# Performance work log

Measured on AMD Instinct MI355X. Metric: run time of the kernel, lower is better.

The kernel has to match this reference:

```python
import jax, jax.numpy as jnp
import numpy as np

N_BIT = 4
GROUP = 128
ALPHA_W = 1.0   # group_size > -1 forces weight alpha to 1.0
ALPHA_A = 0.9   # searched input alpha
TOKENS, D_IN, D_OUT = 2048, 2048, 2048


def _int_grid(n_bit):
    B = n_bit - 1
    v = [0.0] + [float(s * i) for i in range(1, 2 ** B) for s in (1, -1)]
    v = np.sort(np.asarray(v, np.float32)) * (32.0 / 2 ** B)
    return v


def _outlier_grid(n_bit, exp_bit=2, exp_base=5):
    B = n_bit - 1
    mant_bit = B - exp_bit
    vals = []
    for i in range(exp_base, exp_base + 2 ** exp_bit):
        for j in range(2 ** mant_bit):
            if i == exp_base and j == 0:
                continue
            v = 2.0 ** i * (1.0 + 2.0 ** (-mant_bit) * j)
            vals += [v, -v]
    return np.sort(np.asarray(vals, np.float32))


_QG = _int_grid(N_BIT)
MAX_Q = float(_QG.max())              # 28.0 for 4-bit int grid
MERGED_GRID = jnp.asarray(np.concatenate([_QG, _outlier_grid(N_BIT)]))  # [29]


def get_quant(x, alpha, group_size):
    """Faithful jax port of get_quant(): per-group scale, nearest merged-grid
    quantization, roll-based outlier/victim masking, fp16 dequant."""
    org_shape = x.shape
    if group_size == -2:
        t = x.reshape(-1)
        mean, std = t.mean(), t.std(ddof=1)
    else:
        t = x.reshape(-1, group_size) if group_size > 0 else x
        mean = t.mean(axis=1, keepdims=True)
        std = t.std(axis=1, ddof=1, keepdims=True)
    normal_max = jnp.maximum(jnp.abs(mean + 3 * std), jnp.abs(mean - 3 * std))
    scales = normal_max * alpha / MAX_Q
    # nearest grid point over merged quant+outlier grid (the chunk loop in the
    # original is memory-chunking only; math is identical done whole)
    labels = jnp.argmin(jnp.abs((t / scales)[..., None] - MERGED_GRID), axis=-1)
    qf = MERGED_GRID[labels].reshape(-1)
    # victim masking: outliers (|q|>32) steal their paired neighbor's slot
    mask = jnp.abs(qf) > 32.0
    victim_odd = jnp.roll(mask, 1).at[::2].set(False)
    victim_even = jnp.roll(mask & ~victim_odd, -1).at[1::2].set(False)
    qf = jnp.where(victim_odd | victim_even, 0.0, qf)
    if group_size >= -1:
        qf = qf.reshape(t.shape)
    deq = (qf * scales).astype(jnp.float16)
    return deq.reshape(org_shape)


def setup_inputs() -> dict:
    key = jax.random.key(0)
    k1, k2 = jax.random.split(key)
    x = jax.random.normal(k1, (TOKENS, D_IN), dtype=jnp.float32)
    weight = jax.random.normal(k2, (D_OUT, D_IN), dtype=jnp.float32) * 0.02
    return {"x": x, "weight": weight}


def reference(x, weight):
    # runtime path of OliVe_Linear.forward (post-calibration), group_size=128
    w_deq = get_quant(weight, ALPHA_W, GROUP).astype(jnp.float32)
    x_deq = get_quant(x, ALPHA_A, GROUP).astype(jnp.float32)
    return x_deq @ w_deq.T  # [tokens, out_features]
```

## Files before the change

### kernel.cpp

```cpp
#include <hip/hip_runtime.h>
#include <hip/hip_fp16.h>
#include <stdint.h>

#define TOKENS 2048
#define DIM    2048
#define GROUP  128
#define NGK    16

typedef __attribute__((ext_vector_type(4)))  int   i32x4;
typedef __attribute__((ext_vector_type(16))) int   i32x16;
typedef __attribute__((ext_vector_type(4)))  float f32x4;
typedef __attribute__((ext_vector_type(16))) float f32x16;


__device__ __forceinline__ float group32_sum(float v) {
#pragma unroll
  for (int off = 16; off > 0; off >>= 1)
    v += __shfl_xor(v, off, 64);
  return v;
}

__device__ __forceinline__ float nearest_q4(float u) {
  float qi = fminf(fmaxf(rintf(u), -7.f), 7.f);
  float a = fabsf(u);
  float m = a <= 14.f ? 12.f : a <= 20.f ? 16.f : a <= 28.f ? 24.f
          : a <= 40.f ? 32.f : a <= 56.f ? 48.f : a <= 80.f ? 64.f : 96.f;
  float qo = copysignf(m, u);
  return (fabsf(u - qo) < fabsf(u - qi)) ? qo : qi;
}

__global__ __launch_bounds__(256) void quant2_kernel(
    const float* __restrict__ x, const float* __restrict__ w,
    int8_t* __restrict__ q8,
    float* __restrict__ ssxT,
    float* __restrict__ sswT) {
  const int wid  = threadIdx.x >> 6;
  const int lane = threadIdx.x & 63;
  const int l    = lane & 31;
  const int g    = blockIdx.x * 8 + wid * 2 + (lane >> 5);
  const int NG1  = TOKENS * DIM / GROUP;

  const float alpha = (g < NG1) ? 0.9f : 1.0f;
  const float* src  = (g < NG1) ? x : w;
  const int grow    = (g < NG1) ? g : g - NG1;
  const size_t sbase = (size_t)grow * GROUP + l * 4;

  const float4 v = *reinterpret_cast<const float4*>(src + sbase);

  const float mean = group32_sum(v.x + v.y + v.z + v.w) * (1.0f / 128.0f);
  const float d0 = v.x - mean, d1 = v.y - mean, d2 = v.z - mean, d3 = v.w - mean;
  const float var = group32_sum(d0 * d0 + d1 * d1 + d2 * d2 + d3 * d3) *
                    (1.0f / 127.0f);
  const float scale = (fabsf(mean) + 3.0f * sqrtf(var)) * alpha / 28.0f;
  const float rs4 = 0.25f / scale;

  float q0 = nearest_q4(v.x * rs4);
  float q1 = nearest_q4(v.y * rs4);
  float q2 = nearest_q4(v.z * rs4);
  float q3 = nearest_q4(v.w * rs4);
  if (fabsf(q0) > 8.0f)      q1 = 0.0f;
  else if (fabsf(q1) > 8.0f) q0 = 0.0f;
  if (fabsf(q2) > 8.0f)      q3 = 0.0f;
  else if (fabsf(q3) > 8.0f) q2 = 0.0f;

  const int p = ((int)q0 & 255) | (((int)q1 & 255) << 8) |
                (((int)q2 & 255) << 16) | (((int)q3 & 255) << 24);
  reinterpret_cast<int*>(q8)[(size_t)g * 32 + l] = p;

  if (l == 0) {
    const float ss = 4.0f * scale;
    if (g < NG1) ssxT[(grow & 15) * 2048 + (grow >> 4)] = ss;
    else         sswT[(grow & 15) * 2048 + (grow >> 4)] = ss;
  }
}


__device__ __forceinline__ void gload_lds16(const int8_t* g, char* l) {
  __builtin_amdgcn_global_load_lds(
      (__attribute__((address_space(1))) uint32_t*)g,
      (__attribute__((address_space(3))) uint32_t*)l, 16, 0, 0);
}

__global__ __launch_bounds__(256, 2) void gemm_kernel(
    const int8_t* __restrict__ Aq, const int8_t* __restrict__ Bq,
    const float* __restrict__ ssxT, const float* __restrict__ sswT,
    float* __restrict__ C) {
  __shared__ char lds_raw[2 * 24576 + 12288];
  float* ssx_l = (float*)(lds_raw + 49152);
  float* ssw_l = (float*)(lds_raw + 49152 + 8192);

  const int tid  = threadIdx.x;
  const int lane = tid & 63;
  const int wid  = tid >> 6;
  const int wr   = wid >> 1;
  const int wc   = wid & 1;
  const int r31  = lane & 31;
  const int hi   = lane >> 5;

  const int bid = blockIdx.x;
  const int c   = bid & 7;
  const int idx = bid >> 3;
  const int bm  = ((c & 3) << 2) + (idx >> 4);
  const int bn  = ((c >> 2) << 4) + (idx & 15);

  const int8_t* gA = Aq + (size_t)(bm * 128) * DIM;
  const int8_t* gB = Bq + (size_t)(bn * 64) * DIM;

  auto stage = [&](char* buf, int g) {
#pragma unroll
    for (int i = 0; i < 4; ++i) {
      int P   = (i * 256 + tid) * 16;
      int row = P >> 7;
      int cb  = (P & 127) ^ ((row & 7) << 4);
      gload_lds16(gA + (size_t)row * DIM + g * 128 + cb, buf + P);
    }
#pragma unroll
    for (int i = 0; i < 2; ++i) {
      int P   = (i * 256 + tid) * 16;
      int row = P >> 7;
      int cb  = (P & 127) ^ ((row & 7) << 4);
      gload_lds16(gB + (size_t)row * DIM + g * 128 + cb, buf + 16384 + P);
    }
  };

#pragma unroll
  for (int i = 0; i < 2; ++i) {
    int f = (i * 256 + tid) * 4;
    *reinterpret_cast<f32x4*>(&ssx_l[f]) =
        *reinterpret_cast<const f32x4*>(&ssxT[(f >> 7) * 2048 + bm * 128 + (f & 127)]);
  }
  {
    int f = tid * 4;
    *reinterpret_cast<f32x4*>(&ssw_l[f]) =
        *reinterpret_cast<const f32x4*>(&sswT[(f >> 6) * 2048 + bn * 64 + (f & 63)]);
  }
  __syncthreads();

  f32x16 accf[2] = {};
  const i32x16 zacc = {};

  auto compute = [&](const char* buf, int gk) {
    const char* cA = buf;
    const char* cB = buf + 16384;
    i32x16 acci[2];
#pragma unroll
    for (int ks = 0; ks < 4; ++ks) {
      const int cb = ks * 32 + hi * 16;
      i32x4 af[2], bf;
#pragma unroll
      for (int mt = 0; mt < 2; ++mt) {
        int row = wr * 64 + mt * 32 + r31;
        int pc  = cb ^ ((row & 7) << 4);
        af[mt] = *reinterpret_cast<const i32x4*>(cA + (row << 7) + pc);
      }
      {
        int row = wc * 32 + r31;
        int pc  = cb ^ ((row & 7) << 4);
        bf = *reinterpret_cast<const i32x4*>(cB + (row << 7) + pc);
      }
      __builtin_amdgcn_s_setprio(1);
#pragma unroll
      for (int mt = 0; mt < 2; ++mt)
        acci[mt] = __builtin_amdgcn_mfma_i32_32x32x32_i8(
            af[mt], bf, ks == 0 ? zacc : acci[mt], 0, 0, 0);
      __builtin_amdgcn_s_setprio(0);
    }
    const float sw = ssw_l[gk * 64 + wc * 32 + r31];
#pragma unroll
    for (int mt = 0; mt < 2; ++mt)
#pragma unroll
      for (int q = 0; q < 4; ++q) {
        f32x4 sx = *reinterpret_cast<const f32x4*>(
            &ssx_l[gk * 128 + wr * 64 + mt * 32 + 8 * q + 4 * hi]);
#pragma unroll
        for (int e = 0; e < 4; ++e)
          accf[mt][q * 4 + e] += sx[e] * (sw * (float)acci[mt][q * 4 + e]);
      }
  };

  char* S0 = lds_raw;
  char* S1 = lds_raw + 24576;

  stage(S0, 0);
#pragma unroll 2
  for (int j = 0; j < NGK; ++j) {
    if (j + 1 < NGK) {
      stage((j & 1) ? S0 : S1, j + 1);
      asm volatile("s_waitcnt vmcnt(6)" ::: "memory");
    } else {
      asm volatile("s_waitcnt vmcnt(0)" ::: "memory");
    }
    __builtin_amdgcn_s_barrier();
    compute((j & 1) ? S1 : S0, j);
    __builtin_amdgcn_s_barrier();
  }

  const int crow0 = bm * 128 + wr * 64 + 4 * hi;
  const int ccol  = bn * 64 + wc * 32 + r31;
#pragma unroll
  for (int mt = 0; mt < 2; ++mt)
#pragma unroll
    for (int r = 0; r < 16; ++r) {
      int row = crow0 + mt * 32 + (r & 3) + 8 * (r >> 2);
      C[(size_t)row * DIM + ccol] = accf[mt][r];
    }
}


extern "C" void kernel_launch(void* const* d_in, const int* in_sizes, int n_in,
                              void* d_out, int out_size, void* d_ws,
                              size_t ws_size, hipStream_t stream) {
  const float* x = (const float*)d_in[0];
  const float* w = (const float*)d_in[1];
  float* out = (float*)d_out;

  int8_t* qx   = (int8_t*)d_ws;
  int8_t* qw   = qx + (size_t)TOKENS * DIM;
  float*  ssxT = (float*)(qw + (size_t)DIM * DIM);
  float*  sswT = ssxT + NGK * 2048;

  const int ngroups = 2 * TOKENS * DIM / GROUP;
  quant2_kernel<<<ngroups / 8, 256, 0, stream>>>(x, w, qx, ssxT, sswT);

  gemm_kernel<<<512, 256, 0, stream>>>(qx, qw, ssxT, sswT, out);
}
```

Before: 33.94 us.

## Split GEMM K-steps across wave pairs with LDS reduction of partial tiles

Each of the two column waves now covers the full 64-column tile but only half of the K-steps per group (intra-K split). Each wave holds four accumulator tiles and applies the per-group scales to its own partial sums. The partials are then reduced through LDS before one wave writes the output. This reuses each A fragment across two B tiles, cutting LDS reads per MFMA. In exchange it doubles accumulator registers, which may reduce occupancy, and adds an epilogue reduction with barriers. It also drops the unroll-by-2 hint on the main loop.

```diff
diff --git a/kernel.cpp b/kernel.cpp
--- a/kernel.cpp
+++ b/kernel.cpp
@@ -93,7 +93,7 @@
   const int lane = tid & 63;
   const int wid  = tid >> 6;
   const int wr   = wid >> 1;
-  const int wc   = wid & 1;
+  const int wz   = wid & 1;
   const int r31  = lane & 31;
   const int hi   = lane >> 5;
 
@@ -136,36 +136,43 @@
   }
   __syncthreads();
 
-  f32x16 accf[2] = {};
+  f32x16 accf[2][2] = {};
   const i32x16 zacc = {};
 
   auto compute = [&](const char* buf, int gk) {
     const char* cA = buf;
     const char* cB = buf + 16384;
-    i32x16 acci[2];
-#pragma unroll
-    for (int ks = 0; ks < 4; ++ks) {
+    i32x16 acci[2][2];
+#pragma unroll
+    for (int s = 0; s < 2; ++s) {
+      const int ks = wz * 2 + s;
       const int cb = ks * 32 + hi * 16;
-      i32x4 af[2], bf;
+      i32x4 af[2], bf[2];
 #pragma unroll
       for (int mt = 0; mt < 2; ++mt) {
         int row = wr * 64 + mt * 32 + r31;
         int pc  = cb ^ ((row & 7) << 4);
         af[mt] = *reinterpret_cast<const i32x4*>(cA + (row << 7) + pc);
       }
-      {
-        int row = wc * 32 + r31;
+#pragma unroll
+      for (int nt = 0; nt < 2; ++nt) {
+        int row = nt * 32 + r31;
         int pc  = cb ^ ((row & 7) << 4);
-        bf = *reinterpret_cast<const i32x4*>(cB + (row << 7) + pc);
+        bf[nt] = *reinterpret_cast<const i32x4*>(cB + (row << 7) + pc);
       }
       __builtin_amdgcn_s_setprio(1);
 #pragma unroll
       for (int mt = 0; mt < 2; ++mt)
-        acci[mt] = __builtin_amdgcn_mfma_i32_32x32x32_i8(
-            af[mt], bf, ks == 0 ? zacc : acci[mt], 0, 0, 0);
+#pragma unroll
+        for (int nt = 0; nt < 2; ++nt)
+          acci[mt][nt] = __builtin_amdgcn_mfma_i32_32x32x32_i8(
+              af[mt], bf[nt], s == 0 ? zacc : acci[mt][nt], 0, 0, 0);
       __builtin_amdgcn_s_setprio(0);
     }
-    const float sw = ssw_l[gk * 64 + wc * 32 + r31];
+    float sw[2];
+#pragma unroll
+    for (int nt = 0; nt < 2; ++nt)
+      sw[nt] = ssw_l[gk * 64 + nt * 32 + r31];
 #pragma unroll
     for (int mt = 0; mt < 2; ++mt)
 #pragma unroll
@@ -173,8 +180,11 @@
         f32x4 sx = *reinterpret_cast<const f32x4*>(
             &ssx_l[gk * 128 + wr * 64 + mt * 32 + 8 * q + 4 * hi]);
 #pragma unroll
-        for (int e = 0; e < 4; ++e)
-          accf[mt][q * 4 + e] += sx[e] * (sw * (float)acci[mt][q * 4 + e]);
+        for (int nt = 0; nt < 2; ++nt)
+#pragma unroll
+          for (int e = 0; e < 4; ++e)
+            accf[mt][nt][q * 4 + e] +=
+                sx[e] * (sw[nt] * (float)acci[mt][nt][q * 4 + e]);
       }
   };
 
@@ -182,7 +192,6 @@
   char* S1 = lds_raw + 24576;
 
   stage(S0, 0);
-#pragma unroll 2
   for (int j = 0; j < NGK; ++j) {
     if (j + 1 < NGK) {
       stage((j & 1) ? S0 : S1, j + 1);
@@ -195,15 +204,52 @@
     __builtin_amdgcn_s_barrier();
   }
 
-  const int crow0 = bm * 128 + wr * 64 + 4 * hi;
-  const int ccol  = bn * 64 + wc * 32 + r31;
-#pragma unroll
-  for (int mt = 0; mt < 2; ++mt)
-#pragma unroll
-    for (int r = 0; r < 16; ++r) {
-      int row = crow0 + mt * 32 + (r & 3) + 8 * (r >> 2);
-      C[(size_t)row * DIM + ccol] = accf[mt][r];
-    }
+  __syncthreads();
+  float* red = (float*)lds_raw;
+  if (wz == 1) {
+#pragma unroll
+    for (int mt = 0; mt < 2; ++mt)
+#pragma unroll
+      for (int nt = 0; nt < 2; ++nt) {
+        const int t = mt * 2 + nt;
+#pragma unroll
+        for (int q = 0; q < 4; ++q) {
+          f32x4 v;
+          v.x = accf[mt][nt][q * 4 + 0];
+          v.y = accf[mt][nt][q * 4 + 1];
+          v.z = accf[mt][nt][q * 4 + 2];
+          v.w = accf[mt][nt][q * 4 + 3];
+          *reinterpret_cast<f32x4*>(
+              red + (size_t)((wr * 16 + t * 4 + q) * 64 + lane) * 4) = v;
+        }
+      }
+  }
+  __syncthreads();
+  if (wz == 0) {
+    const int crow0 = bm * 128 + wr * 64 + 4 * hi;
+    const int ccol0 = bn * 64 + r31;
+#pragma unroll
+    for (int mt = 0; mt < 2; ++mt)
+#pragma unroll
+      for (int nt = 0; nt < 2; ++nt) {
+        const int t = mt * 2 + nt;
+#pragma unroll
+        for (int q = 0; q < 4; ++q) {
+          f32x4 v = *reinterpret_cast<const f32x4*>(
+              red + (size_t)((wr * 16 + t * 4 + q) * 64 + lane) * 4);
+          accf[mt][nt][q * 4 + 0] += v.x;
+          accf[mt][nt][q * 4 + 1] += v.y;
+          accf[mt][nt][q * 4 + 2] += v.z;
+          accf[mt][nt][q * 4 + 3] += v.w;
+        }
+#pragma unroll
+        for (int r = 0; r < 16; ++r) {
+          int row = crow0 + mt * 32 + (r & 3) + 8 * (r >> 2);
+          int col = ccol0 + nt * 32;
+          C[(size_t)row * DIM + col] = accf[mt][nt][r];
+        }
+      }
+  }
 }
 
 
```

Measured after the change: 37.74 us. +11.2%, slower.

## Triple-buffer GEMM LDS pipeline and store group scales as fp16

Applied to the files above, without the earlier changes.

Changes the int8 GEMM main loop from double to triple buffering, issuing loads two K-groups ahead and waiting with vmcnt(12). This hides more global-load latency. To fit three 24 KB stages in LDS, the per-group scales are stored and staged as fp16 instead of fp32, which halves the scale footprint. The costs are rounding error in the scales and higher LDS use per block (about 78 KB), which may limit occupancy under the 2-block launch bound.

```diff
diff --git a/kernel.cpp b/kernel.cpp
--- a/kernel.cpp
+++ b/kernel.cpp
@@ -7,6 +7,9 @@
 #define GROUP  128
 #define NGK    16
 
+typedef _Float16 half_t;
+typedef __attribute__((ext_vector_type(4)))  _Float16 f16x4;
+typedef __attribute__((ext_vector_type(8)))  _Float16 f16x8;
 typedef __attribute__((ext_vector_type(4)))  int   i32x4;
 typedef __attribute__((ext_vector_type(16))) int   i32x16;
 typedef __attribute__((ext_vector_type(4)))  float f32x4;
@@ -32,8 +35,8 @@
 __global__ __launch_bounds__(256) void quant2_kernel(
     const float* __restrict__ x, const float* __restrict__ w,
     int8_t* __restrict__ q8,
-    float* __restrict__ ssxT,
-    float* __restrict__ sswT) {
+    half_t* __restrict__ ssxT,
+    half_t* __restrict__ sswT) {
   const int wid  = threadIdx.x >> 6;
   const int lane = threadIdx.x & 63;
   const int l    = lane & 31;
@@ -68,7 +71,7 @@
   reinterpret_cast<int*>(q8)[(size_t)g * 32 + l] = p;
 
   if (l == 0) {
-    const float ss = 4.0f * scale;
+    const half_t ss = (half_t)(4.0f * scale);
     if (g < NG1) ssxT[(grow & 15) * 2048 + (grow >> 4)] = ss;
     else         sswT[(grow & 15) * 2048 + (grow >> 4)] = ss;
   }
@@ -83,11 +86,11 @@
 
 __global__ __launch_bounds__(256, 2) void gemm_kernel(
     const int8_t* __restrict__ Aq, const int8_t* __restrict__ Bq,
-    const float* __restrict__ ssxT, const float* __restrict__ sswT,
+    const half_t* __restrict__ ssxT, const half_t* __restrict__ sswT,
     float* __restrict__ C) {
-  __shared__ char lds_raw[2 * 24576 + 12288];
-  float* ssx_l = (float*)(lds_raw + 49152);
-  float* ssw_l = (float*)(lds_raw + 49152 + 8192);
+  __shared__ char lds_raw[3 * 24576 + 6144];
+  half_t* ssx_l = (half_t*)(lds_raw + 73728);
+  half_t* ssw_l = (half_t*)(lds_raw + 73728 + 4096);
 
   const int tid  = threadIdx.x;
   const int lane = tid & 63;
@@ -123,16 +126,15 @@
     }
   };
 
-#pragma unroll
-  for (int i = 0; i < 2; ++i) {
-    int f = (i * 256 + tid) * 4;
-    *reinterpret_cast<f32x4*>(&ssx_l[f]) =
-        *reinterpret_cast<const f32x4*>(&ssxT[(f >> 7) * 2048 + bm * 128 + (f & 127)]);
-  }
   {
-    int f = tid * 4;
-    *reinterpret_cast<f32x4*>(&ssw_l[f]) =
-        *reinterpret_cast<const f32x4*>(&sswT[(f >> 6) * 2048 + bn * 64 + (f & 63)]);
+    int f = tid * 8;
+    *reinterpret_cast<f16x8*>(&ssx_l[f]) =
+        *reinterpret_cast<const f16x8*>(&ssxT[(f >> 7) * 2048 + bm * 128 + (f & 127)]);
+  }
+  if (tid < 128) {
+    int f = tid * 8;
+    *reinterpret_cast<f16x8*>(&ssw_l[f]) =
+        *reinterpret_cast<const f16x8*>(&sswT[(f >> 6) * 2048 + bn * 64 + (f & 63)]);
   }
   __syncthreads();
 
@@ -165,35 +167,50 @@
             af[mt], bf, ks == 0 ? zacc : acci[mt], 0, 0, 0);
       __builtin_amdgcn_s_setprio(0);
     }
-    const float sw = ssw_l[gk * 64 + wc * 32 + r31];
+    const float sw = (float)ssw_l[gk * 64 + wc * 32 + r31];
 #pragma unroll
     for (int mt = 0; mt < 2; ++mt)
 #pragma unroll
       for (int q = 0; q < 4; ++q) {
-        f32x4 sx = *reinterpret_cast<const f32x4*>(
+        f16x4 sxh = *reinterpret_cast<const f16x4*>(
             &ssx_l[gk * 128 + wr * 64 + mt * 32 + 8 * q + 4 * hi]);
 #pragma unroll
         for (int e = 0; e < 4; ++e)
-          accf[mt][q * 4 + e] += sx[e] * (sw * (float)acci[mt][q * 4 + e]);
+          accf[mt][q * 4 + e] +=
+              (float)sxh[e] * (sw * (float)acci[mt][q * 4 + e]);
       }
   };
 
   char* S0 = lds_raw;
   char* S1 = lds_raw + 24576;
+  char* S2 = lds_raw + 49152;
 
   stage(S0, 0);
-#pragma unroll 2
-  for (int j = 0; j < NGK; ++j) {
-    if (j + 1 < NGK) {
-      stage((j & 1) ? S0 : S1, j + 1);
+  stage(S1, 1);
+
+  auto iter = [&](int j, const char* cbuf, char* sbuf) {
+    if (j <= 13) {
+      stage(sbuf, j + 2);
+      asm volatile("s_waitcnt vmcnt(12)" ::: "memory");
+    } else if (j == 14) {
       asm volatile("s_waitcnt vmcnt(6)" ::: "memory");
     } else {
       asm volatile("s_waitcnt vmcnt(0)" ::: "memory");
     }
     __builtin_amdgcn_s_barrier();
-    compute((j & 1) ? S1 : S0, j);
+    compute(cbuf, j);
     __builtin_amdgcn_s_barrier();
-  }
+  };
+
+  for (int t = 0; t < 12; t += 3) {
+    iter(t + 0, S0, S2);
+    iter(t + 1, S1, S0);
+    iter(t + 2, S2, S1);
+  }
+  iter(12, S0, S2);
+  iter(13, S1, S0);
+  iter(14, S2, S1);
+  iter(15, S0, S2);
 
   const int crow0 = bm * 128 + wr * 64 + 4 * hi;
   const int ccol  = bn * 64 + wc * 32 + r31;
@@ -216,8 +233,8 @@
 
   int8_t* qx   = (int8_t*)d_ws;
   int8_t* qw   = qx + (size_t)TOKENS * DIM;
-  float*  ssxT = (float*)(qw + (size_t)DIM * DIM);
-  float*  sswT = ssxT + NGK * 2048;
+  half_t* ssxT = (half_t*)(qw + (size_t)DIM * DIM);
+  half_t* sswT = ssxT + NGK * 2048;
 
   const int ngroups = 2 * TOKENS * DIM / GROUP;
   quant2_kernel<<<ngroups / 8, 256, 0, stream>>>(x, w, qx, ssxT, sswT);
```

Result: slower. 35.51 us (+4.6%).

## Software-pipeline group-scale epilogue behind next group's MFMAs, batch LDS fragment loads

Applied to the files above, without the earlier changes.

Restructures the GEMM main loop so each k-group's int32 accumulators are scaled and added into the float accumulators during the following iteration, alternating between two accumulator sets. It also loads all four k-slices of A/B fragments from LDS up front before issuing the MFMAs. The aim is to overlap the dequant-scale FMAs and LDS fragment latency with MFMA execution instead of serializing them. This costs more registers (two i32x16 pairs, cached scales, 12 fragment vectors), which may pressure occupancy at launch bounds of 2 waves per SIMD.

```diff
diff --git a/kernel.cpp b/kernel.cpp
--- a/kernel.cpp
+++ b/kernel.cpp
@@ -139,51 +139,24 @@
   f32x16 accf[2] = {};
   const i32x16 zacc = {};
 
-  auto compute = [&](const char* buf, int gk) {
-    const char* cA = buf;
-    const char* cB = buf + 16384;
-    i32x16 acci[2];
-#pragma unroll
-    for (int ks = 0; ks < 4; ++ks) {
-      const int cb = ks * 32 + hi * 16;
-      i32x4 af[2], bf;
-#pragma unroll
-      for (int mt = 0; mt < 2; ++mt) {
-        int row = wr * 64 + mt * 32 + r31;
-        int pc  = cb ^ ((row & 7) << 4);
-        af[mt] = *reinterpret_cast<const i32x4*>(cA + (row << 7) + pc);
-      }
-      {
-        int row = wc * 32 + r31;
-        int pc  = cb ^ ((row & 7) << 4);
-        bf = *reinterpret_cast<const i32x4*>(cB + (row << 7) + pc);
-      }
-      __builtin_amdgcn_s_setprio(1);
-#pragma unroll
-      for (int mt = 0; mt < 2; ++mt)
-        acci[mt] = __builtin_amdgcn_mfma_i32_32x32x32_i8(
-            af[mt], bf, ks == 0 ? zacc : acci[mt], 0, 0, 0);
-      __builtin_amdgcn_s_setprio(0);
-    }
-    const float sw = ssw_l[gk * 64 + wc * 32 + r31];
-#pragma unroll
-    for (int mt = 0; mt < 2; ++mt)
-#pragma unroll
-      for (int q = 0; q < 4; ++q) {
-        f32x4 sx = *reinterpret_cast<const f32x4*>(
-            &ssx_l[gk * 128 + wr * 64 + mt * 32 + 8 * q + 4 * hi]);
-#pragma unroll
-        for (int e = 0; e < 4; ++e)
-          accf[mt][q * 4 + e] += sx[e] * (sw * (float)acci[mt][q * 4 + e]);
-      }
-  };
-
   char* S0 = lds_raw;
   char* S1 = lds_raw + 24576;
 
-  stage(S0, 0);
-#pragma unroll 2
-  for (int j = 0; j < NGK; ++j) {
+  float sw_c = 0.0f;
+  f32x4 sx_c[2][4];
+
+  auto apply = [&](const i32x16 prev[2]) {
+#pragma unroll
+    for (int mt = 0; mt < 2; ++mt)
+#pragma unroll
+      for (int q = 0; q < 4; ++q)
+#pragma unroll
+        for (int e = 0; e < 4; ++e)
+          accf[mt][q * 4 + e] +=
+              sx_c[mt][q][e] * (sw_c * (float)prev[mt][q * 4 + e]);
+  };
+
+  auto step = [&](int j, i32x16 out[2], const i32x16 prev[2]) {
     if (j + 1 < NGK) {
       stage((j & 1) ? S0 : S1, j + 1);
       asm volatile("s_waitcnt vmcnt(6)" ::: "memory");
@@ -191,9 +164,54 @@
       asm volatile("s_waitcnt vmcnt(0)" ::: "memory");
     }
     __builtin_amdgcn_s_barrier();
-    compute((j & 1) ? S1 : S0, j);
+    const char* buf = (j & 1) ? S1 : S0;
+    const char* cA = buf;
+    const char* cB = buf + 16384;
+
+    i32x4 af[4][2], bf[4];
+#pragma unroll
+    for (int ks = 0; ks < 4; ++ks) {
+      const int cb = ks * 32 + hi * 16;
+#pragma unroll
+      for (int mt = 0; mt < 2; ++mt) {
+        int row = wr * 64 + mt * 32 + r31;
+        int pc  = cb ^ ((row & 7) << 4);
+        af[ks][mt] = *reinterpret_cast<const i32x4*>(cA + (row << 7) + pc);
+      }
+      int row = wc * 32 + r31;
+      int pc  = cb ^ ((row & 7) << 4);
+      bf[ks] = *reinterpret_cast<const i32x4*>(cB + (row << 7) + pc);
+    }
+
+    if (j > 0) apply(prev);
+
+    sw_c = ssw_l[j * 64 + wc * 32 + r31];
+#pragma unroll
+    for (int mt = 0; mt < 2; ++mt)
+#pragma unroll
+      for (int q = 0; q < 4; ++q)
+        sx_c[mt][q] = *reinterpret_cast<const f32x4*>(
+            &ssx_l[j * 128 + wr * 64 + mt * 32 + 8 * q + 4 * hi]);
+
+    __builtin_amdgcn_s_setprio(1);
+#pragma unroll
+    for (int ks = 0; ks < 4; ++ks)
+#pragma unroll
+      for (int mt = 0; mt < 2; ++mt)
+        out[mt] = __builtin_amdgcn_mfma_i32_32x32x32_i8(
+            af[ks][mt], bf[ks], ks == 0 ? zacc : out[mt], 0, 0, 0);
+    __builtin_amdgcn_s_setprio(0);
     __builtin_amdgcn_s_barrier();
-  }
+  };
+
+  i32x16 acciA[2], acciB[2];
+
+  stage(S0, 0);
+  for (int jj = 0; jj < NGK; jj += 2) {
+    step(jj + 0, acciA, acciB);
+    step(jj + 1, acciB, acciA);
+  }
+  apply(acciB);
 
   const int crow0 = bm * 128 + wr * 64 + 4 * hi;
   const int ccol  = bn * 64 + wc * 32 + r31;
```

Measured after the change: 34.63 us. +2.0%, slower.
